# Kernel optimization log

Measured on AMD Instinct MI355X. Metric: run time of the kernel, lower is better.

## Reference

```python
import jax, jax.numpy as jnp
import numpy as np

TEMPERATURE = 0.1
EPS = 1e-12  # matches torch F.normalize eps


def _l2_normalize(x, axis=-1):
    n = jnp.sqrt(jnp.sum(x * x, axis=axis, keepdims=True))
    return x / jnp.maximum(n, EPS)


def setup_inputs() -> dict:
    key = jax.random.key(0)
    k1, k2, k3 = jax.random.split(key, 3)
    B, K, D, M = 128, 256, 256, 4
    local_vectors = jax.random.normal(k1, (B, K, D), dtype=jnp.float32)
    prototypes = jax.random.normal(k2, (K * M, D, 1, 1), dtype=jnp.float32)
    concepts_gt = jax.random.randint(k3, (B, K), 0, 2, dtype=jnp.int32)
    return {
        "local_vectors": local_vectors,
        "prototypes": prototypes,
        "concepts_gt": concepts_gt,
        "num_prototypes_per_concept": M,
    }


def reference(local_vectors, prototypes, concepts_gt, num_prototypes_per_concept):
    B, K, D = local_vectors.shape
    M = num_prototypes_per_concept
    protos = prototypes.reshape(K * M, D)  # squeeze(-1).squeeze(-1)
    ln = _l2_normalize(local_vectors)      # (B, K, D)
    pn = _l2_normalize(protos)             # (K*M, D)

    # similarities for every (b, k) query against all prototypes in one GEMM
    sims = jnp.einsum('bkd,pd->bkp', ln, pn) / TEMPERATURE  # (B, K, K*M)

    # logsumexp over all prototypes (shared across the M positives of a concept)
    lse = jax.nn.logsumexp(sims, axis=-1)  # (B, K)

    # sum of positive similarities: prototypes k*M..(k+1)*M-1 for concept k
    # diagonal over the two K axes, summed over m
    pos_sum = jnp.einsum('bkkm->bk', sims.reshape(B, K, K, M))  # (B, K)

    mask = (concepts_gt == 1).astype(sims.dtype)  # (B, K)
    Mf = jnp.asarray(M, sims.dtype)
    total = jnp.sum(mask * (Mf * lse - pos_sum))
    count = Mf * jnp.sum(mask)
    return jnp.where(count > 0, total / jnp.maximum(count, 1.0), jnp.zeros((), sims.dtype))
```

## Files before the change

### kernel.cpp

```cpp
#include <hip/hip_runtime.h>
#include <hip/hip_bf16.h>
#include <stdint.h>

#define KC   256
#define DD   256
#define NPROT 1024
#define NQ   32768

#define OFF_NSEL 0
#define OFF_TOT  8
#define OFF_TICK 16
#define OFF_SEL  256
#define OFF_PN   131328
#define OFF_QN   655616
#define QSLAB    1048576
#define OFF_ACC  17432832
#define ACC_STRIDE 32768

#define LN2F    0.69314718055994531f
#define C10L2E  14.426950408889634f

typedef __bf16 bf16x8 __attribute__((ext_vector_type(8)));
typedef float  f32x16 __attribute__((ext_vector_type(16)));

static __device__ __forceinline__ unsigned short f2bf(float x) {
  __hip_bfloat16 h = __float2bfloat16(x);
  return __builtin_bit_cast(unsigned short, h);
}

__global__ __launch_bounds__(512) void prep_k(const int* __restrict__ gt,
                                              const float* __restrict__ lv,
                                              const float* __restrict__ protos,
                                              unsigned char* __restrict__ ws) {
  const int blk = blockIdx.x;
  const int tid = threadIdx.x;

  if (blk < 128) {
    const int wv = tid >> 6, lane = tid & 63;
    const int r = blk * 8 + wv;
    const float4 v = ((const float4*)protos)[r * 64 + lane];
    float ss = v.x*v.x + v.y*v.y + v.z*v.z + v.w*v.w;
#pragma unroll
    for (int m = 1; m < 64; m <<= 1) ss += __shfl_xor(ss, m, 64);
    const float sc = C10L2E / fmaxf(sqrtf(ss), 1e-12f);
    uint2 p;
    p.x = (unsigned)f2bf(v.x * sc) | ((unsigned)f2bf(v.y * sc) << 16);
    p.y = (unsigned)f2bf(v.z * sc) | ((unsigned)f2bf(v.w * sc) << 16);
    *(uint2*)(ws + OFF_PN + (lane >> 2) * 32768 + r * 32 + (lane & 3) * 8) = p;
    return;
  }

  __shared__ int wcnt[8], wpre[8];
  __shared__ int sbase, btot;
  __shared__ int list[512];

  const int wv   = tid >> 6, lane = tid & 63;
  const int idx  = (blk - 128) * 512 + tid;

  const int selme = (gt[idx] == 1);
  const unsigned long long bal = __ballot(selme);
  if (lane == 0) wcnt[wv] = __popcll(bal);
  __syncthreads();
  if (tid == 0) {
    int tot = 0;
#pragma unroll
    for (int u = 0; u < 8; ++u) { wpre[u] = tot; tot += wcnt[u]; }
    btot  = tot;
    sbase = atomicAdd((int*)(ws + OFF_NSEL), tot);
  }
  __syncthreads();

  const int rank = __popcll(bal & ((1ull << lane) - 1ull));
  if (selme) {
    const int loc = wpre[wv] + rank;
    list[loc] = idx;
    ((int*)(ws + OFF_SEL))[sbase + loc] = idx;
  }
  __syncthreads();

  const int grp = tid >> 4, sub = tid & 15;
  const int nr  = btot, sb = sbase;
  for (int r = grp; r < nr; r += 32) {
    const int qi   = list[r];
    const int slot = sb + r;
    float4 vv[4];
#pragma unroll
    for (int u = 0; u < 4; ++u) vv[u] = ((const float4*)lv)[qi * 64 + u * 16 + sub];
    float ss = 0.0f;
#pragma unroll
    for (int u = 0; u < 4; ++u)
      ss += vv[u].x*vv[u].x + vv[u].y*vv[u].y + vv[u].z*vv[u].z + vv[u].w*vv[u].w;
#pragma unroll
    for (int m = 1; m < 16; m <<= 1) ss += __shfl_xor(ss, m, 64);
    const float sc = 1.0f / fmaxf(sqrtf(ss), 1e-12f);
#pragma unroll
    for (int u = 0; u < 4; ++u) {
      uint2 p;
      p.x = (unsigned)f2bf(vv[u].x * sc) | ((unsigned)f2bf(vv[u].y * sc) << 16);
      p.y = (unsigned)f2bf(vv[u].z * sc) | ((unsigned)f2bf(vv[u].w * sc) << 16);
      *(uint2*)(ws + OFF_QN + (u * 4 + (sub >> 2)) * QSLAB + slot * 32 + (sub & 3) * 8) = p;
    }
  }
}

__global__ __launch_bounds__(256) void main_k(unsigned char* __restrict__ ws) {
  __shared__ __align__(16) unsigned char Aq[64 * 512];

  const int tid  = threadIdx.x;
  const int w    = tid >> 6;
  const int lane = tid & 63;
  const int hi   = lane >> 5;
  const int l31  = lane & 31;

  const int tile = (int)(blockIdx.x & 511);
  const int c    = (int)(blockIdx.x >> 9);

  const int n_sel = *(const int*)(ws + OFF_NSEL);
  const int base  = tile * 64;
  if (base >= n_sel) return;
  const int* sel = (const int*)(ws + OFF_SEL);

  int valid[2], kqr[2];
#pragma unroll
  for (int j = 0; j < 2; ++j) {
    const int slot = base + j * 32 + l31;
    valid[j] = slot < n_sel;
    const int q = valid[j] ? sel[slot] : sel[base];
    kqr[j] = q & (KC - 1);
  }

  const unsigned char* pn0 = ws + OFF_PN + (c * 256 + w * 64 + l31) * 32 + hi * 16;
  const unsigned char* pn1 = pn0 + 32 * 32;

  bf16x8 pa0[4], pa1[4];
#pragma unroll
  for (int p = 0; p < 4; ++p) {
    pa0[p] = *(const bf16x8*)(pn0 + p * 32768);
    pa1[p] = *(const bf16x8*)(pn1 + p * 32768);
  }

  const unsigned char* qn = ws + OFF_QN;
  const int last = n_sel - 1;
#pragma unroll
  for (int i = 0; i < 4; ++i) {
    const int unit = i * 256 + tid;
    const int s = unit >> 6, r = unit & 63;
    const int slot = min(base + r, last);
    const unsigned char* src = qn + s * QSLAB + slot * 32;
    const uint4 d0 = *(const uint4*)(src);
    const uint4 d1 = *(const uint4*)(src + 16);
    const int swz = ((r & 7) << 4) ^ (((r >> 3) & 3) << 7);
    *(uint4*)(Aq + r * 512 + ((s * 32) ^ swz))      = d0;
    *(uint4*)(Aq + r * 512 + ((s * 32 + 16) ^ swz)) = d1;
  }
  __syncthreads();

  f32x16 acc[2][2];
#pragma unroll
  for (int i = 0; i < 2; ++i)
#pragma unroll
    for (int j = 0; j < 2; ++j)
#pragma unroll
      for (int t = 0; t < 16; ++t) acc[i][j][t] = 0.0f;

  const int bswz = ((l31 & 7) << 4) ^ (((l31 >> 3) & 3) << 7);

#pragma unroll
  for (int k = 0; k < 16; ++k) {
    const bf16x8 a0 = pa0[k & 3];
    const bf16x8 a1 = pa1[k & 3];
    pa0[k & 3] = *(const bf16x8*)(pn0 + ((k + 4) & 15) * 32768);
    pa1[k & 3] = *(const bf16x8*)(pn1 + ((k + 4) & 15) * 32768);
    const int bc = (k * 32 + hi * 16) ^ bswz;
    const bf16x8 b0 = *(const bf16x8*)(Aq + l31 * 512 + bc);
    const bf16x8 b1 = *(const bf16x8*)(Aq + (32 + l31) * 512 + bc);
    acc[0][0] = __builtin_amdgcn_mfma_f32_32x32x16_bf16(a0, b0, acc[0][0], 0, 0, 0);
    acc[0][1] = __builtin_amdgcn_mfma_f32_32x32x16_bf16(a0, b1, acc[0][1], 0, 0, 0);
    acc[1][0] = __builtin_amdgcn_mfma_f32_32x32x16_bf16(a1, b0, acc[1][0], 0, 0, 0);
    acc[1][1] = __builtin_amdgcn_mfma_f32_32x32x16_bf16(a1, b1, acc[1][1], 0, 0, 0);
  }

  float l_acc[2] = {0.f, 0.f}, p_acc[2] = {0.f, 0.f};
#pragma unroll
  for (int i = 0; i < 2; ++i) {
    const int r4base = c * 64 + w * 16 + i * 8 + hi;
#pragma unroll
    for (int j = 0; j < 2; ++j) {
      float l4[4] = {0.f, 0.f, 0.f, 0.f};
      float p4[4] = {0.f, 0.f, 0.f, 0.f};
#pragma unroll
      for (int g = 0; g < 4; ++g) {
        const float pm = (r4base + 2 * g == kqr[j]) ? 1.0f : 0.0f;
#pragma unroll
        for (int t = 0; t < 4; ++t) {
          const float y = acc[i][j][g * 4 + t];
          l4[t] += __builtin_amdgcn_exp2f(y);
          p4[t] = fmaf(pm, y, p4[t]);
        }
      }
      l_acc[j] += (l4[0] + l4[1]) + (l4[2] + l4[3]);
      p_acc[j] += (p4[0] + p4[1]) + (p4[2] + p4[3]);
    }
  }

#pragma unroll
  for (int j = 0; j < 2; ++j) {
    l_acc[j] += __shfl_xor(l_acc[j], 32, 64);
    p_acc[j] += __shfl_xor(p_acc[j], 32, 64);
  }
  if (hi == 0) {
    float2* accb = (float2*)(ws + OFF_ACC) + (c * 4 + w) * ACC_STRIDE;
#pragma unroll
    for (int j = 0; j < 2; ++j) {
      if (valid[j]) {
        const int slot = base + j * 32 + l31;
        float2 v2; v2.x = l_acc[j]; v2.y = p_acc[j];
        accb[slot] = v2;
      }
    }
  }
}

__global__ __launch_bounds__(256) void finish_k(unsigned char* __restrict__ ws,
                                                float* __restrict__ out) {
  __shared__ float accs[4];
  const int n_sel = *(const int*)(ws + OFF_NSEL);
  const int i = blockIdx.x * 256 + threadIdx.x;
  float contrib = 0.0f;
  if (i < n_sel) {
    const float2* a = (const float2*)(ws + OFF_ACC);
    float L = 0.0f, P = 0.0f;
#pragma unroll
    for (int u = 0; u < 16; ++u) {
      const float2 v = a[u * ACC_STRIDE + i];
      L += v.x; P += v.y;
    }
    contrib = LN2F * (4.0f * __builtin_amdgcn_logf(L) - P);
  }
#pragma unroll
  for (int m = 1; m < 64; m <<= 1) contrib += __shfl_xor(contrib, m, 64);
  if ((threadIdx.x & 63) == 0) accs[threadIdx.x >> 6] = contrib;
  __syncthreads();
  if (threadIdx.x == 0) {
    atomicAdd((float*)(ws + OFF_TOT), (accs[0] + accs[1]) + (accs[2] + accs[3]));
    __threadfence();
    const int t = atomicAdd((int*)(ws + OFF_TICK), 1);
    if (t == 127) {
      const float total = atomicAdd((float*)(ws + OFF_TOT), 0.0f);
      out[0] = (n_sel > 0) ? total / (4.0f * (float)n_sel) : 0.0f;
    }
  }
}

extern "C" void kernel_launch(void* const* d_in, const int* in_sizes, int n_in,
                              void* d_out, int out_size, void* d_ws, size_t ws_size,
                              hipStream_t stream) {
  const float* lv     = (const float*)d_in[0];
  const float* protos = (const float*)d_in[1];
  const int*   gt     = (const int*)d_in[2];
  (void)in_sizes; (void)n_in; (void)out_size; (void)ws_size;
  unsigned char* ws = (unsigned char*)d_ws;

  hipMemsetAsync(d_ws, 0, 256, stream);
  prep_k<<<192, 512, 0, stream>>>(gt, lv, protos, ws);
  main_k<<<2048, 256, 0, stream>>>(ws);
  finish_k<<<128, 256, 0, stream>>>(ws, (float*)d_out);
}
```

Measured before the change: 36.97 us.

## Fuse final reduction into main kernel via per-tile and global tickets

Removes the separate finish kernel launch. Each main block first reduces its four wave partials in shared memory and writes one partial per prototype chunk. A per-tile atomic ticket then lets the last of the four chunk blocks compute the log terms and add them to the global total, and a global ticket lets the last tile write the output. This saves a kernel launch and shrinks the partial buffer, at the cost of extra atomics and barriers in the main kernel's tail.

```diff
diff --git a/kernel.cpp b/kernel.cpp
--- a/kernel.cpp
+++ b/kernel.cpp
@@ -7,15 +7,15 @@
 #define NPROT 1024
 #define NQ   32768
 
-#define OFF_NSEL 0
-#define OFF_TOT  8
-#define OFF_TICK 16
-#define OFF_SEL  256
-#define OFF_PN   131328
-#define OFF_QN   655616
-#define QSLAB    1048576
-#define OFF_ACC  17432832
-#define ACC_STRIDE 32768
+#define OFF_TOT   0
+#define OFF_GTICK 8
+#define OFF_NSEL  16
+#define OFF_TTICK 256
+#define OFF_SEL   4096
+#define OFF_PN    135168
+#define OFF_QN    659456
+#define QSLAB     1048576
+#define OFF_ACC   17436672
 
 #define LN2F    0.69314718055994531f
 #define C10L2E  14.426950408889634f
@@ -103,8 +103,10 @@
   }
 }
 
-__global__ __launch_bounds__(256) void main_k(unsigned char* __restrict__ ws) {
+__global__ __launch_bounds__(256) void main_k(unsigned char* __restrict__ ws,
+                                              float* __restrict__ out) {
   __shared__ __align__(16) unsigned char Aq[64 * 512];
+  __shared__ int lastf;
 
   const int tid  = threadIdx.x;
   const int w    = tid >> 6;
@@ -117,15 +119,17 @@
 
   const int n_sel = *(const int*)(ws + OFF_NSEL);
   const int base  = tile * 64;
-  if (base >= n_sel) return;
+  if (base >= n_sel) {
+    if (blockIdx.x == 0 && tid == 0) out[0] = 0.0f;
+    return;
+  }
   const int* sel = (const int*)(ws + OFF_SEL);
 
-  int valid[2], kqr[2];
+  int kqr[2];
 #pragma unroll
   for (int j = 0; j < 2; ++j) {
     const int slot = base + j * 32 + l31;
-    valid[j] = slot < n_sel;
-    const int q = valid[j] ? sel[slot] : sel[base];
+    const int q = (slot < n_sel) ? sel[slot] : sel[base];
     kqr[j] = q & (KC - 1);
   }
 
@@ -208,46 +212,60 @@
     l_acc[j] += __shfl_xor(l_acc[j], 32, 64);
     p_acc[j] += __shfl_xor(p_acc[j], 32, 64);
   }
+
+  __syncthreads();
+  float* red = (float*)Aq;
   if (hi == 0) {
-    float2* accb = (float2*)(ws + OFF_ACC) + (c * 4 + w) * ACC_STRIDE;
 #pragma unroll
     for (int j = 0; j < 2; ++j) {
-      if (valid[j]) {
-        const int slot = base + j * 32 + l31;
-        float2 v2; v2.x = l_acc[j]; v2.y = p_acc[j];
-        accb[slot] = v2;
+      const int s = j * 32 + l31;
+      red[(w * 64 + s) * 2]     = l_acc[j];
+      red[(w * 64 + s) * 2 + 1] = p_acc[j];
+    }
+  }
+  __syncthreads();
+  if (tid < 64) {
+    float L = 0.f, P = 0.f;
+#pragma unroll
+    for (int u = 0; u < 4; ++u) {
+      L += red[(u * 64 + tid) * 2];
+      P += red[(u * 64 + tid) * 2 + 1];
+    }
+    float2 v2; v2.x = L; v2.y = P;
+    ((float2*)(ws + OFF_ACC))[c * 32768 + base + tid] = v2;
+    __threadfence();
+  }
+  __syncthreads();
+
+  if (tid == 0) {
+    __threadfence();
+    lastf = (atomicAdd((int*)(ws + OFF_TTICK) + tile, 1) == 3);
+  }
+  __syncthreads();
+  if (!lastf) return;
+
+  float contrib = 0.0f;
+  if (tid < 64) {
+    const int slot = base + tid;
+    if (slot < n_sel) {
+      float L = 0.f, P = 0.f;
+#pragma unroll
+      for (int u = 0; u < 4; ++u) {
+        float* p2 = (float*)(ws + OFF_ACC) + (u * 32768 + slot) * 2;
+        L += atomicAdd(p2, 0.0f);
+        P += atomicAdd(p2 + 1, 0.0f);
       }
-    }
-  }
-}
-
-__global__ __launch_bounds__(256) void finish_k(unsigned char* __restrict__ ws,
-                                                float* __restrict__ out) {
-  __shared__ float accs[4];
-  const int n_sel = *(const int*)(ws + OFF_NSEL);
-  const int i = blockIdx.x * 256 + threadIdx.x;
-  float contrib = 0.0f;
-  if (i < n_sel) {
-    const float2* a = (const float2*)(ws + OFF_ACC);
-    float L = 0.0f, P = 0.0f;
-#pragma unroll
-    for (int u = 0; u < 16; ++u) {
-      const float2 v = a[u * ACC_STRIDE + i];
-      L += v.x; P += v.y;
-    }
-    contrib = LN2F * (4.0f * __builtin_amdgcn_logf(L) - P);
-  }
-#pragma unroll
-  for (int m = 1; m < 64; m <<= 1) contrib += __shfl_xor(contrib, m, 64);
-  if ((threadIdx.x & 63) == 0) accs[threadIdx.x >> 6] = contrib;
-  __syncthreads();
-  if (threadIdx.x == 0) {
-    atomicAdd((float*)(ws + OFF_TOT), (accs[0] + accs[1]) + (accs[2] + accs[3]));
-    __threadfence();
-    const int t = atomicAdd((int*)(ws + OFF_TICK), 1);
-    if (t == 127) {
-      const float total = atomicAdd((float*)(ws + OFF_TOT), 0.0f);
-      out[0] = (n_sel > 0) ? total / (4.0f * (float)n_sel) : 0.0f;
+      contrib = LN2F * (4.0f * __builtin_amdgcn_logf(L) - P);
+    }
+#pragma unroll
+    for (int m = 1; m < 64; m <<= 1) contrib += __shfl_xor(contrib, m, 64);
+    if (tid == 0) {
+      atomicAdd((float*)(ws + OFF_TOT), contrib);
+      __threadfence();
+      const int g = atomicAdd((int*)(ws + OFF_GTICK), 1);
+      const int n_tiles = (n_sel + 63) >> 6;
+      if (g == n_tiles - 1)
+        out[0] = atomicAdd((float*)(ws + OFF_TOT), 0.0f) / (4.0f * (float)n_sel);
     }
   }
 }
@@ -261,8 +279,7 @@
   (void)in_sizes; (void)n_in; (void)out_size; (void)ws_size;
   unsigned char* ws = (unsigned char*)d_ws;
 
-  hipMemsetAsync(d_ws, 0, 256, stream);
+  hipMemsetAsync(d_ws, 0, 4096, stream);
   prep_k<<<192, 512, 0, stream>>>(gt, lv, protos, ws);
-  main_k<<<2048, 256, 0, stream>>>(ws);
-  finish_k<<<128, 256, 0, stream>>>(ws, (float*)d_out);
-}
+  main_k<<<2048, 256, 0, stream>>>(ws, (float*)d_out);
+}
```

Result: slower. 70.95 us (+91.9%).

## Split query normalization out of prep kernel into a separate wide kernel

Applied to the files above, without the earlier changes.

Query gathering and L2 normalization move out of the compaction kernel, where only 64 blocks handled about 16K selected rows, into a new qnorm_k kernel launched with 512 blocks. Each block of the new kernel normalizes up to 64 compacted slots. The aim is to spread the memory-bound normalization over more CUs for more parallelism. The cost is an extra kernel launch and the serialization between launches.

```diff
diff --git a/kernel.cpp b/kernel.cpp
--- a/kernel.cpp
+++ b/kernel.cpp
@@ -29,7 +29,6 @@
 }
 
 __global__ __launch_bounds__(512) void prep_k(const int* __restrict__ gt,
-                                              const float* __restrict__ lv,
                                               const float* __restrict__ protos,
                                               unsigned char* __restrict__ ws) {
   const int blk = blockIdx.x;
@@ -51,8 +50,7 @@
   }
 
   __shared__ int wcnt[8], wpre[8];
-  __shared__ int sbase, btot;
-  __shared__ int list[512];
+  __shared__ int sbase;
 
   const int wv   = tid >> 6, lane = tid & 63;
   const int idx  = (blk - 128) * 512 + tid;
@@ -65,24 +63,28 @@
     int tot = 0;
 #pragma unroll
     for (int u = 0; u < 8; ++u) { wpre[u] = tot; tot += wcnt[u]; }
-    btot  = tot;
     sbase = atomicAdd((int*)(ws + OFF_NSEL), tot);
   }
   __syncthreads();
 
   const int rank = __popcll(bal & ((1ull << lane) - 1ull));
-  if (selme) {
-    const int loc = wpre[wv] + rank;
-    list[loc] = idx;
-    ((int*)(ws + OFF_SEL))[sbase + loc] = idx;
-  }
-  __syncthreads();
-
-  const int grp = tid >> 4, sub = tid & 15;
-  const int nr  = btot, sb = sbase;
-  for (int r = grp; r < nr; r += 32) {
-    const int qi   = list[r];
-    const int slot = sb + r;
+  if (selme)
+    ((int*)(ws + OFF_SEL))[sbase + wpre[wv] + rank] = idx;
+}
+
+__global__ __launch_bounds__(256) void qnorm_k(const float* __restrict__ lv,
+                                               unsigned char* __restrict__ ws) {
+  const int n_sel = *(const int*)(ws + OFF_NSEL);
+  const int base  = (int)blockIdx.x * 64;
+  if (base >= n_sel) return;
+  const int* sel = (const int*)(ws + OFF_SEL);
+
+  const int grp = threadIdx.x >> 4, sub = threadIdx.x & 15;
+#pragma unroll
+  for (int t = 0; t < 4; ++t) {
+    const int slot = base + grp * 4 + t;
+    if (slot >= n_sel) break;
+    const int qi = sel[slot];
     float4 vv[4];
 #pragma unroll
     for (int u = 0; u < 4; ++u) vv[u] = ((const float4*)lv)[qi * 64 + u * 16 + sub];
@@ -262,7 +264,8 @@
   unsigned char* ws = (unsigned char*)d_ws;
 
   hipMemsetAsync(d_ws, 0, 256, stream);
-  prep_k<<<192, 512, 0, stream>>>(gt, lv, protos, ws);
+  prep_k<<<192, 512, 0, stream>>>(gt, protos, ws);
+  qnorm_k<<<512, 256, 0, stream>>>(lv, ws);
   main_k<<<2048, 256, 0, stream>>>(ws);
   finish_k<<<128, 256, 0, stream>>>(ws, (float*)d_out);
 }
```

Measured after the change: 35.53 us. 3.9% less time.
